# Kernel optimization log

Hardware: AMD Instinct MI355X
Metric: run time of the kernel (lower is better)

Reference implementation:

```python
import math
import jax, jax.numpy as jnp
import numpy as np

N_HEADS = 16


def setup_inputs() -> dict:
    key = jax.random.key(0)
    qkv = jax.random.normal(key, (4, 3072, 2048), dtype=jnp.float32)
    return {"qkv": qkv}


def reference(qkv) -> jnp.ndarray:
    bs, width, length = qkv.shape
    assert width % (3 * N_HEADS) == 0
    ch = width // (3 * N_HEADS)
    # [bs*H, 3*ch, T] -> q, k, v each [bs*H, ch, T]
    qkv_r = qkv.reshape(bs * N_HEADS, 3 * ch, length)
    q, k, v = qkv_r[:, :ch], qkv_r[:, ch:2 * ch], qkv_r[:, 2 * ch:]
    scale = 1.0 / math.sqrt(math.sqrt(ch))
    # scores: [bs*H, T, T]
    weight = jnp.einsum('bct,bcs->bts', q * scale, k * scale)
    weight = jax.nn.softmax(weight.astype(jnp.float32), axis=-1).astype(weight.dtype)
    a = jnp.einsum('bts,bcs->bct', weight, v)  # [bs*H, ch, T]
    return a.reshape(bs, N_HEADS * ch, length)
```

## Files before the change

kernel.cpp:

```cpp
#include <hip/hip_runtime.h>
#include <hip/hip_bf16.h>
#include <cstdint>
#include <cstddef>

typedef short bf16x8 __attribute__((ext_vector_type(8)));
typedef float f32x16 __attribute__((ext_vector_type(16)));
typedef unsigned int uint2v __attribute__((ext_vector_type(2)));

#if __has_builtin(__builtin_amdgcn_exp2f)
#define EXP2F(x) __builtin_amdgcn_exp2f(x)
#else
#define EXP2F(x) exp2f(x)
#endif

#define QSCALE 0.18033688011112043f

__device__ __forceinline__ short f2bf(float f) {
  union { __hip_bfloat16 b; short s; } u;
  u.b = __float2bfloat16(f);
  return u.s;
}

__device__ __forceinline__ unsigned int fbits(float f) {
  union { float f; unsigned int u; } x; x.f = f; return x.u;
}
__device__ __forceinline__ float bfloat(unsigned int u) {
  union { unsigned int u; float f; } x; x.u = u; return x.f;
}

__device__ __forceinline__ unsigned int pkbf(float a, float b) {
  return ((fbits(a) + 0x8000u) >> 16) | ((fbits(b) + 0x8000u) & 0xFFFF0000u);
}

__device__ __forceinline__ float fmax_x32(float v) {
  const uint2v r = __builtin_amdgcn_permlane32_swap(fbits(v), fbits(v),
                                                    false, false);
  return fmaxf(bfloat(r[0]), bfloat(r[1]));
}
__device__ __forceinline__ float fadd_x32(float v) {
  const uint2v r = __builtin_amdgcn_permlane32_swap(fbits(v), fbits(v),
                                                    false, false);
  return bfloat(r[0]) + bfloat(r[1]);
}

__device__ __forceinline__ void gload16(const short* g, char* l) {
  __builtin_amdgcn_global_load_lds(
      (const __attribute__((address_space(1))) void*)g,
      (__attribute__((address_space(3))) void*)l, 16, 0, 0);
}

__global__ __launch_bounds__(256, 4) void qkv_prep_kernel(
    const float* __restrict__ qkv, short* __restrict__ Kt,
    short* __restrict__ Vb) {
  const int bh = blockIdx.x >> 5;
  const int s0 = (blockIdx.x & 31) << 6;
  const int tid = threadIdx.x;
  const int row = tid >> 2;
  const int part = tid & 3;
  __shared__ float lds[64 * 65];

  const size_t qb = (size_t)bh * (192 * 2048);

  {
    const float* src = qkv + qb + (size_t)(64 + row) * 2048 + s0 + part * 16;
#pragma unroll
    for (int k4 = 0; k4 < 4; ++k4) {
      float4 v = ((const float4*)src)[k4];
      float* p = &lds[row * 65 + part * 16 + k4 * 4];
      p[0] = v.x; p[1] = v.y; p[2] = v.z; p[3] = v.w;
    }
  }
  __syncthreads();
  {
    bf16x8 o0, o1;
#pragma unroll
    for (int k = 0; k < 8; ++k) o0[k] = f2bf(lds[(part * 16 + k) * 65 + row]);
#pragma unroll
    for (int k = 0; k < 8; ++k) o1[k] = f2bf(lds[(part * 16 + 8 + k) * 65 + row]);
    short* dst = Kt + ((size_t)bh * 2048 + s0 + row) * 64 + part * 16;
    *(bf16x8*)dst = o0;
    *(bf16x8*)(dst + 8) = o1;
  }
  {
    const float* src = qkv + qb + (size_t)(128 + row) * 2048 + s0 + part * 16;
    float a[16];
#pragma unroll
    for (int k4 = 0; k4 < 4; ++k4) {
      float4 v = ((const float4*)src)[k4];
      a[k4 * 4 + 0] = v.x; a[k4 * 4 + 1] = v.y;
      a[k4 * 4 + 2] = v.z; a[k4 * 4 + 3] = v.w;
    }
    bf16x8 o0, o1;
#pragma unroll
    for (int k = 0; k < 8; ++k) { o0[k] = f2bf(a[k]); o1[k] = f2bf(a[8 + k]); }
    short* dst = Vb + ((size_t)bh * 64 + row) * 2048 + s0 + part * 16;
    *(bf16x8*)dst = o0;
    *(bf16x8*)(dst + 8) = o1;
  }
}

__global__ __launch_bounds__(256, 4) void attn32_kernel(
    const float* __restrict__ qkv, const short* __restrict__ Kt,
    const short* __restrict__ Vb, float* __restrict__ out) {
  const int bid = blockIdx.x;
  const int vid = (bid & 7) * 128 + (bid >> 3);
  const int bh = vid >> 4;
  const int tblk = vid & 15;
  const int tid = threadIdx.x;
  const int wv = tid >> 6;
  const int lane = tid & 63;
  const int tl = lane & 31;
  const int hi = lane >> 5;
  const int t0w = tblk * 128 + wv * 32;

  __shared__ __align__(16) char smem[32768];

  const size_t qb = (size_t)bh * (192 * 2048);
  bf16x8 qf[4];
#pragma unroll
  for (int kc = 0; kc < 4; ++kc) {
#pragma unroll
    for (int j = 0; j < 8; ++j) {
      const int c = kc * 16 + hi * 8 + j;
      qf[kc][j] = f2bf(qkv[qb + (size_t)c * 2048 + t0w + tl] * QSCALE);
    }
  }

  f32x16 zv;
#pragma unroll
  for (int r = 0; r < 16; ++r) zv[r] = 0.f;

  f32x16 acc[2];
#pragma unroll
  for (int cb = 0; cb < 2; ++cb) acc[cb] = zv;

  float mrun = -1e30f;
  float lsum = 0.f;

  const int rsw = (tl & 7) * 16;
  int off[2][4];
#pragma unroll
  for (int x = 0; x < 2; ++x)
#pragma unroll
    for (int j = 0; j < 4; ++j)
      off[x][j] = (x * 32 + tl) * 128 + ((j * 32 + hi * 16) ^ rsw);

  const int r8 = lane >> 3;
  const int sl = lane & 7;
  const int row0 = wv * 16 + r8;
  const int row1 = wv * 16 + 8 + r8;
  const short* kg0 = Kt + (size_t)bh * (2048 * 64) + (size_t)row0 * 64 +
                     ((sl ^ (row0 & 7)) * 8);
  const short* kg1 = Kt + (size_t)bh * (2048 * 64) + (size_t)row1 * 64 +
                     ((sl ^ (row1 & 7)) * 8);
  const short* vg0 = Vb + ((size_t)bh * 64 + row0) * 2048 +
                     ((sl ^ (row0 & 7)) * 8);
  const short* vg1 = Vb + ((size_t)bh * 64 + row1) * 2048 +
                     ((sl ^ (row1 & 7)) * 8);
  const int ldK0 = (wv * 16) * 128;
  const int ldK1 = (wv * 16 + 8) * 128;

  {
    gload16(kg0, smem + ldK0);
    gload16(kg1, smem + ldK1);
    gload16(vg0, smem + 8192 + ldK0);
    gload16(vg1, smem + 8192 + ldK1);
  }

#pragma unroll 2
  for (int ch = 0; ch < 32; ++ch) {
    char* const Kls = smem + (ch & 1) * 16384;
    char* const Vls = Kls + 8192;

    __syncthreads();

    if (ch < 31) {
      char* const Knx = smem + ((ch + 1) & 1) * 16384;
      const size_t ka = (size_t)(ch + 1) * 4096;
      const int va = (ch + 1) * 64;
      gload16(kg0 + ka, Knx + ldK0);
      gload16(kg1 + ka, Knx + ldK1);
      gload16(vg0 + va, Knx + 8192 + ldK0);
      gload16(vg1 + va, Knx + 8192 + ldK1);
    }

    f32x16 lg[2];
#pragma unroll
    for (int st = 0; st < 2; ++st) {
      bf16x8 ka = *(const bf16x8*)(Kls + off[st][0]);
      lg[st] = __builtin_amdgcn_mfma_f32_32x32x16_bf16(ka, qf[0], zv, 0, 0, 0);
#pragma unroll
      for (int kc = 1; kc < 4; ++kc) {
        ka = *(const bf16x8*)(Kls + off[st][kc]);
        lg[st] = __builtin_amdgcn_mfma_f32_32x32x16_bf16(ka, qf[kc], lg[st],
                                                         0, 0, 0);
      }
    }

    float w[11];
#pragma unroll
    for (int i = 0; i < 5; ++i)
      w[i] = fmaxf(fmaxf(lg[0][3 * i], lg[0][3 * i + 1]), lg[0][3 * i + 2]);
    w[5] = fmaxf(fmaxf(lg[0][15], lg[1][0]), lg[1][1]);
#pragma unroll
    for (int i = 0; i < 4; ++i)
      w[6 + i] = fmaxf(fmaxf(lg[1][3 * i + 2], lg[1][3 * i + 3]),
                       lg[1][3 * i + 4]);
    w[10] = fmaxf(lg[1][14], lg[1][15]);
    const float x0 = fmaxf(fmaxf(w[0], w[1]), w[2]);
    const float x1 = fmaxf(fmaxf(w[3], w[4]), w[5]);
    const float x2 = fmaxf(fmaxf(w[6], w[7]), w[8]);
    const float x3 = fmaxf(w[9], w[10]);
    float cm = fmax_x32(fmaxf(fmaxf(x0, x1), fmaxf(x2, x3)));
    if (!__all(cm <= mrun + 8.0f)) {
      const float nm = fmaxf(mrun, cm);
      const float fac = EXP2F(mrun - nm);
      mrun = nm;
      lsum *= fac;
#pragma unroll
      for (int cb = 0; cb < 2; ++cb)
#pragma unroll
        for (int r = 0; r < 16; ++r) acc[cb][r] *= fac;
    }

    float ps = 0.f;
#pragma unroll
    for (int st = 0; st < 2; ++st) {
#pragma unroll
      for (int r = 0; r < 16; ++r) lg[st][r] = EXP2F(lg[st][r] - mrun);
#pragma unroll
      for (int r = 0; r < 8; ++r) ps += lg[st][2 * r] + lg[st][2 * r + 1];
    }
    lsum += ps;

    bf16x8 pa[4];
#pragma unroll
    for (int st = 0; st < 2; ++st) {
#pragma unroll
      for (int kl = 0; kl < 2; ++kl) {
        const unsigned int p0a = pkbf(lg[st][8 * kl + 0], lg[st][8 * kl + 1]);
        const unsigned int p0b = pkbf(lg[st][8 * kl + 2], lg[st][8 * kl + 3]);
        const unsigned int p1a = pkbf(lg[st][8 * kl + 4], lg[st][8 * kl + 5]);
        const unsigned int p1b = pkbf(lg[st][8 * kl + 6], lg[st][8 * kl + 7]);
        const unsigned int sa = hi ? p0a : p1a;
        const unsigned int sb = hi ? p0b : p1b;
        const unsigned int ra = __shfl_xor(sa, 32);
        const unsigned int rb = __shfl_xor(sb, 32);
        union { unsigned int w[4]; bf16x8 v; } u;
        u.w[0] = hi ? ra : p0a;
        u.w[1] = hi ? rb : p0b;
        u.w[2] = hi ? p1a : ra;
        u.w[3] = hi ? p1b : rb;
        pa[st * 2 + kl] = u.v;
      }
    }

#pragma unroll
    for (int cb = 0; cb < 2; ++cb) {
#pragma unroll
      for (int ks = 0; ks < 4; ++ks) {
        const bf16x8 vb = *(const bf16x8*)(Vls + off[cb][ks]);
        acc[cb] = __builtin_amdgcn_mfma_f32_32x32x16_bf16(vb, pa[ks], acc[cb],
                                                          0, 0, 0);
      }
    }
  }

  const float ls = fadd_x32(lsum);
  const float inv = 1.0f / ls;
#pragma unroll
  for (int cb = 0; cb < 2; ++cb) {
#pragma unroll
    for (int r = 0; r < 16; ++r) {
      const int c = cb * 32 + (r & 3) + 8 * (r >> 2) + 4 * hi;
      out[((size_t)bh * 64 + c) * 2048 + t0w + tl] = acc[cb][r] * inv;
    }
  }
}

extern "C" void kernel_launch(void* const* d_in, const int* in_sizes, int n_in,
                              void* d_out, int out_size, void* d_ws,
                              size_t ws_size, hipStream_t stream) {
  (void)in_sizes; (void)n_in; (void)out_size;
  const float* qkv = (const float*)d_in[0];
  float* out = (float*)d_out;
  const size_t kv_elems = (size_t)64 * 2048 * 64;
  if (ws_size < kv_elems * 2 * sizeof(short)) return;
  short* Kt = (short*)d_ws;
  short* Vb = Kt + kv_elems;
  hipLaunchKernelGGL(qkv_prep_kernel, dim3(2048), dim3(256), 0, stream,
                     qkv, Kt, Vb);
  hipLaunchKernelGGL(attn32_kernel, dim3(1024), dim3(256), 0, stream,
                     qkv, Kt, Vb, out);
}
```

Baseline: 122.6 us.

## Double attention block to 8 waves covering 256 queries sharing K/V tiles

Each attention workgroup now has 512 threads (8 waves) and covers 256 query positions instead of 128, so every K/V chunk staged in LDS is reused by twice as many waves. Each thread now issues one K and one V async load per chunk instead of two of each, halving per-thread load work and total global K/V traffic. The grid shrinks to 512 blocks. Per-CU occupancy and barrier cost change with the bigger block, and the launch bound of 512x4 may tighten the register budget.

```diff
diff --git a/kernel.cpp b/kernel.cpp
--- a/kernel.cpp
+++ b/kernel.cpp
@@ -99,19 +99,19 @@
   }
 }
 
-__global__ __launch_bounds__(256, 4) void attn32_kernel(
+__global__ __launch_bounds__(512, 4) void attn32_kernel(
     const float* __restrict__ qkv, const short* __restrict__ Kt,
     const short* __restrict__ Vb, float* __restrict__ out) {
   const int bid = blockIdx.x;
-  const int vid = (bid & 7) * 128 + (bid >> 3);
-  const int bh = vid >> 4;
-  const int tblk = vid & 15;
+  const int vid = (bid & 7) * 64 + (bid >> 3);
+  const int bh = vid >> 3;
+  const int tblk = vid & 7;
   const int tid = threadIdx.x;
   const int wv = tid >> 6;
   const int lane = tid & 63;
   const int tl = lane & 31;
   const int hi = lane >> 5;
-  const int t0w = tblk * 128 + wv * 32;
+  const int t0w = tblk * 256 + wv * 32;
 
   __shared__ __align__(16) char smem[32768];
 
@@ -145,27 +145,16 @@
     for (int j = 0; j < 4; ++j)
       off[x][j] = (x * 32 + tl) * 128 + ((j * 32 + hi * 16) ^ rsw);
 
-  const int r8 = lane >> 3;
-  const int sl = lane & 7;
-  const int row0 = wv * 16 + r8;
-  const int row1 = wv * 16 + 8 + r8;
-  const short* kg0 = Kt + (size_t)bh * (2048 * 64) + (size_t)row0 * 64 +
-                     ((sl ^ (row0 & 7)) * 8);
-  const short* kg1 = Kt + (size_t)bh * (2048 * 64) + (size_t)row1 * 64 +
-                     ((sl ^ (row1 & 7)) * 8);
-  const short* vg0 = Vb + ((size_t)bh * 64 + row0) * 2048 +
-                     ((sl ^ (row0 & 7)) * 8);
-  const short* vg1 = Vb + ((size_t)bh * 64 + row1) * 2048 +
-                     ((sl ^ (row1 & 7)) * 8);
-  const int ldK0 = (wv * 16) * 128;
-  const int ldK1 = (wv * 16 + 8) * 128;
-
-  {
-    gload16(kg0, smem + ldK0);
-    gload16(kg1, smem + ldK1);
-    gload16(vg0, smem + 8192 + ldK0);
-    gload16(vg1, smem + 8192 + ldK1);
-  }
+  const int srow = tid >> 3;
+  const int sl = tid & 7;
+  const short* kg = Kt + (size_t)bh * (2048 * 64) + (size_t)srow * 64 +
+                    ((sl ^ (srow & 7)) * 8);
+  const short* vg = Vb + ((size_t)bh * 64 + srow) * 2048 +
+                    ((sl ^ (srow & 7)) * 8);
+  const int ldb = wv * 1024;
+
+  gload16(kg, smem + ldb);
+  gload16(vg, smem + 8192 + ldb);
 
 #pragma unroll 2
   for (int ch = 0; ch < 32; ++ch) {
@@ -176,12 +165,8 @@
 
     if (ch < 31) {
       char* const Knx = smem + ((ch + 1) & 1) * 16384;
-      const size_t ka = (size_t)(ch + 1) * 4096;
-      const int va = (ch + 1) * 64;
-      gload16(kg0 + ka, Knx + ldK0);
-      gload16(kg1 + ka, Knx + ldK1);
-      gload16(vg0 + va, Knx + 8192 + ldK0);
-      gload16(vg1 + va, Knx + 8192 + ldK1);
+      gload16(kg + (size_t)(ch + 1) * 4096, Knx + ldb);
+      gload16(vg + (ch + 1) * 64, Knx + 8192 + ldb);
     }
 
     f32x16 lg[2];
@@ -290,6 +275,6 @@
   short* Vb = Kt + kv_elems;
   hipLaunchKernelGGL(qkv_prep_kernel, dim3(2048), dim3(256), 0, stream,
                      qkv, Kt, Vb);
-  hipLaunchKernelGGL(attn32_kernel, dim3(1024), dim3(256), 0, stream,
+  hipLaunchKernelGGL(attn32_kernel, dim3(512), dim3(512), 0, stream,
                      qkv, Kt, Vb, out);
 }
```

Result: faster. 116.9 us (-4.7%).
